# Kernel tuning notes

Measured on AMD Instinct MI355X. Metric: run time of the kernel, lower is better.

Reference implementation:

```python
import jax, jax.numpy as jnp
import numpy as np

K = 75        # kpoints
L = 8         # number of labels (output_dim)


def _knn_nonconformity(q, t, train_label, k=K, num_labels=L):
    """Brute-force kNN (Euclidean) + distance-weighted nonconformity.
    q: [B, D] queries; t: [N, D] train bank; train_label: [N] int.
    Returns [B, num_labels]: for each class i, sum of 1/dist over the k
    nearest neighbors whose label != i (0 weight for zero distance)."""
    # squared distances [B, N]
    d2 = (jnp.sum(q * q, axis=1, keepdims=True)
          - 2.0 * q @ t.T
          + jnp.sum(t * t, axis=1)[None, :])
    d2 = jnp.maximum(d2, 0.0)
    neg_top, idx = jax.lax.top_k(-d2, k)          # k smallest d2
    dist = jnp.sqrt(jnp.maximum(-neg_top, 0.0))    # [B, k]
    safe = jnp.where(dist > 0, dist, 1.0)
    w = jnp.where(dist > 0, 1.0 / safe, 0.0)       # [B, k]
    mismatch = 1.0 - jax.nn.one_hot(train_label[idx], num_labels, dtype=w.dtype)  # [B,k,L]
    return jnp.einsum('bk,bkl->bl', w, mismatch)


def setup_inputs() -> dict:
    key = jax.random.key(0)
    ks = jax.random.split(key, 12)
    B, N, D, H, C = 1024, 50000, 83, 128, 10000
    s = lambda fan_in: 1.0 / np.sqrt(fan_in)
    return {
        'x': jax.random.normal(ks[0], (B, D), jnp.float32),
        'train_x': jax.random.normal(ks[1], (N, D), jnp.float32),
        'train_label': jax.random.randint(ks[2], (N,), 0, L, jnp.int32),
        'cali': jax.random.uniform(ks[3], (C,), jnp.float32) * 50.0,
        'W1': jax.random.normal(ks[4], (D, H), jnp.float32) * s(D),
        'b1': jnp.zeros((H,), jnp.float32),
        'W2': jax.random.normal(ks[5], (H, H), jnp.float32) * s(H),
        'b2': jnp.zeros((H,), jnp.float32),
        'W3': jax.random.normal(ks[6], (H, H), jnp.float32) * s(H),
        'b3': jnp.zeros((H,), jnp.float32),
        'W4': jax.random.normal(ks[7], (H, L), jnp.float32) * s(H),
        'b4': jnp.zeros((L,), jnp.float32),
    }


def reference(x, train_x, train_label, cali, W1, b1, W2, b2, W3, b3, W4, b4):
    relu = jax.nn.relu
    # query-side MLP (inference: dropout inactive)
    h1 = relu(x @ W1 + b1)
    h2 = relu(h1 @ W2 + b2)
    h3 = relu(h2 @ W3 + b3)
    out = jax.nn.softmax(h3 @ W4 + b4, axis=-1)
    # train-side feature banks (what each kNTree was fit on)
    t1 = relu(train_x @ W1 + b1)
    t2 = relu(t1 @ W2 + b2)
    t3 = relu(t2 @ W3 + b3)
    t4 = jax.nn.softmax(t3 @ W4 + b4, axis=-1)
    # per-layer nonconformity [B, L], summed across the 5 layers
    total = (_knn_nonconformity(x, train_x, train_label)
             + _knn_nonconformity(h1, t1, train_label)
             + _knn_nonconformity(h2, t2, train_label)
             + _knn_nonconformity(h3, t3, train_label)
             + _knn_nonconformity(out, t4, train_label))
    # empirical p-value: fraction of calibration scores >= total nonconformity
    counts = jnp.sum(cali[None, None, :] >= total[:, :, None], axis=-1)  # [B, L]
    return counts.astype(jnp.float32) / cali.shape[0]
```

## Files before the change

### kernel.cpp

```cpp
#include <hip/hip_runtime.h>
#include <math.h>

#define KNN 75
#define NL 8
#define NB 1024
#define NT 50000
#define NT_PAD 50048
#define NCALI 10000
#define KC 32
#define TT 128
#define NTB 391
#define SLOTS 16
#define CAP 6144
#define NSUB 2048
#define NSB 16
#define SSTRIDE 24
#define SOFF 11
#define RSEL 32

#define PB_Q    384
#define PB_BANK 18750
#define PB_W1   48
#define PB_W23  64
#define PREP_BLOCKS (PB_Q+PB_BANK+PB_W1+2*PB_W23)

typedef __attribute__((ext_vector_type(8))) short bf16x8;
typedef __attribute__((ext_vector_type(4))) float f32x4;

__device__ __forceinline__ int swz(int c){ return c + ((c>>5)<<2); }

__device__ __forceinline__ unsigned short f2bf_rn(float x){
  unsigned u = __float_as_uint(x);
  unsigned r = (u + 0x7FFFu + ((u>>16)&1u)) >> 16;
  return (unsigned short)r;
}
__device__ __forceinline__ float bf2f(unsigned short h){
  return __uint_as_float(((unsigned)h)<<16);
}
__device__ __forceinline__ bf16x8 ld8(const unsigned short* p){
  return *(const bf16x8*)p;
}
__device__ __forceinline__ void gl_lds16(const unsigned short* g, unsigned short* l){
  __builtin_amdgcn_global_load_lds(
      (const __attribute__((address_space(1))) void*)g,
      (__attribute__((address_space(3))) void*)l, 16, 0, 0);
}

__device__ __forceinline__ void pad_one(const float* __restrict__ in,
                                        float* __restrict__ out, int M,
                                        int Din, int Dout, int idx){
  if (idx >= M*Dout) return;
  int r = idx / Dout, c = idx - r*Dout;
  out[idx] = (c < Din) ? in[r*Din + c] : 0.f;
}
__device__ __forceinline__ void wsplit_one(const float* __restrict__ W, int kreal,
                                           int dp, unsigned short* __restrict__ WtH,
                                           unsigned short* __restrict__ WtL, int idx){
  int n = idx / dp, k = idx - n*dp;
  float v = (k < kreal) ? W[(size_t)k*128 + n] : 0.f;
  unsigned short h = f2bf_rn(v);
  WtH[idx] = h;
  WtL[idx] = f2bf_rn(v - bf2f(h));
}
__global__ void prep_k(const float* __restrict__ x, float* __restrict__ xq0,
                       const float* __restrict__ txr, float* __restrict__ tbA,
                       const float* __restrict__ W1, unsigned short* wt1H, unsigned short* wt1L,
                       const float* __restrict__ W2, unsigned short* wt2H, unsigned short* wt2L,
                       const float* __restrict__ W3, unsigned short* wt3H, unsigned short* wt3L){
  int b = blockIdx.x, tid = threadIdx.x;
  if (b < PB_Q){
    pad_one(x, xq0, NB, 83, 96, b*256 + tid);
  } else if (b < PB_Q + PB_BANK){
    pad_one(txr, tbA, NT, 83, 96, (b-PB_Q)*256 + tid);
  } else if (b < PB_Q + PB_BANK + PB_W1){
    wsplit_one(W1, 83, 96,  wt1H, wt1L, (b-PB_Q-PB_BANK)*256 + tid);
  } else if (b < PB_Q + PB_BANK + PB_W1 + PB_W23){
    wsplit_one(W2, 128, 128, wt2H, wt2L, (b-PB_Q-PB_BANK-PB_W1)*256 + tid);
  } else {
    wsplit_one(W3, 128, 128, wt3H, wt3L, (b-PB_Q-PB_BANK-PB_W1-PB_W23)*256 + tid);
  }
}

__device__ __forceinline__ void qmlp_layer(
    const float* __restrict__ srcG, int lda,
    float (*H)[132], float (*As)[132], float (*Bs)[148],
    int kchunks, int kreal,
    const float* __restrict__ W, const float* __restrict__ bias,
    float* __restrict__ OutG, int rowBase, int tid)
{
  int r0 = (tid>>4)*8, c0 = (tid&15)*8;
  float acc[8][8];
  #pragma unroll
  for (int i=0;i<8;i++)
    #pragma unroll
    for (int j=0;j<8;j++) acc[i][j]=0.f;

  for (int kc=0;kc<kchunks;kc++){
    { int rr = tid>>3, k4=(tid&7)*4;
      #pragma unroll
      for (int i=0;i<4;i++){
        int row = rr + i*32;
        float4 v;
        if (srcG) v = *(const float4*)&srcG[(size_t)(rowBase+row)*lda + kc*KC + k4];
        else      v = *(const float4*)&H[row][kc*KC + k4];
        As[k4+0][row]=v.x; As[k4+1][row]=v.y; As[k4+2][row]=v.z; As[k4+3][row]=v.w;
      }
    }
    { int kk=tid>>5, c4=(tid&31)*4;
      #pragma unroll
      for (int i=0;i<4;i++){
        int k = kk + i*8, gk = kc*KC + k;
        float4 v = make_float4(0.f,0.f,0.f,0.f);
        if (gk < kreal) v = *(const float4*)&W[(size_t)gk*128 + c4];
        *(float4*)&Bs[k][swz(c4)] = v;
      }
    }
    __syncthreads();
    #pragma unroll 4
    for (int k=0;k<KC;k++){
      float4 a0 = *(const float4*)&As[k][r0];
      float4 a1 = *(const float4*)&As[k][r0+4];
      float4 b0 = *(const float4*)&Bs[k][swz(c0)];
      float4 b1 = *(const float4*)&Bs[k][swz(c0+4)];
      float av[8] = {a0.x,a0.y,a0.z,a0.w,a1.x,a1.y,a1.z,a1.w};
      float bv[8] = {b0.x,b0.y,b0.z,b0.w,b1.x,b1.y,b1.z,b1.w};
      #pragma unroll
      for (int i=0;i<8;i++)
        #pragma unroll
        for (int j=0;j<8;j++) acc[i][j] += av[i]*bv[j];
    }
    __syncthreads();
  }
  float bb[8];
  #pragma unroll
  for (int j=0;j<8;j++) bb[j]=bias[c0+j];
  #pragma unroll
  for (int i=0;i<8;i++){
    int row = r0 + i;
    float o[8];
    #pragma unroll
    for (int j=0;j<8;j++){ float v=acc[i][j]+bb[j]; o[j]=v>0.f?v:0.f; }
    *(float4*)&H[row][c0]   = make_float4(o[0],o[1],o[2],o[3]);
    *(float4*)&H[row][c0+4] = make_float4(o[4],o[5],o[6],o[7]);
    *(float4*)&OutG[(size_t)(rowBase+row)*128 + c0]   = make_float4(o[0],o[1],o[2],o[3]);
    *(float4*)&OutG[(size_t)(rowBase+row)*128 + c0+4] = make_float4(o[4],o[5],o[6],o[7]);
  }
  __syncthreads();
}

__global__ __launch_bounds__(256) void qmlp_k(
    const float* __restrict__ xq0,
    const float* __restrict__ W1, const float* __restrict__ b1,
    const float* __restrict__ W2, const float* __restrict__ b2,
    const float* __restrict__ W3, const float* __restrict__ b3,
    const float* __restrict__ W4, const float* __restrict__ b4,
    float* __restrict__ xq1, float* __restrict__ xq2, float* __restrict__ xq3,
    float* __restrict__ xq4)
{
  __shared__ float As[KC][132];
  __shared__ float Bs[KC][148];
  __shared__ float H[128][132];
  int tid = threadIdx.x;
  int rowBase = blockIdx.x*128;

  qmlp_layer(xq0, 96, H, As, Bs, 3, 83,  W1, b1, xq1, rowBase, tid);
  qmlp_layer(nullptr, 0, H, As, Bs, 4, 128, W2, b2, xq2, rowBase, tid);
  qmlp_layer(nullptr, 0, H, As, Bs, 4, 128, W3, b3, xq3, rowBase, tid);

  float* W4s = (float*)Bs;
  for (int i=tid;i<1024;i+=256) W4s[i]=W4[i];
  __syncthreads();
  if (tid < 128){
    int row = rowBase + tid;
    float v[8];
    #pragma unroll
    for (int c=0;c<8;c++) v[c]=b4[c];
    for (int k=0;k<128;k++){
      float a = H[tid][k];
      #pragma unroll
      for (int c=0;c<8;c++) v[c] += a*W4s[k*8+c];
    }
    float m=-1e30f;
    #pragma unroll
    for (int c=0;c<8;c++) m = v[c]>m ? v[c] : m;
    float s=0.f;
    #pragma unroll
    for (int c=0;c<8;c++){ v[c]=__expf(v[c]-m); s+=v[c]; }
    float inv=1.f/s;
    float* p = &xq4[(size_t)row*32];
    #pragma unroll
    for (int c=0;c<8;c++) p[c]=v[c]*inv;
    #pragma unroll
    for (int j=8;j<32;j++) p[j]=0.f;
  }
}

__global__ void mlp8sm_k(const float* __restrict__ A, const float* __restrict__ W4,
                         const float* __restrict__ b4, float* __restrict__ Out, int M){
  __shared__ float Ws[128*8];
  int tid = threadIdx.x;
  for (int i=tid;i<1024;i+=256) Ws[i]=W4[i];
  __syncthreads();
  int r = blockIdx.x*32 + (tid>>3), c = tid&7;
  if (r >= M) return;
  const float* a = &A[(size_t)r*128];
  float acc = b4[c];
  #pragma unroll 16
  for (int k=0;k<128;k++) acc += a[k]*Ws[k*8+c];
  int lane = tid & 63, base = lane & ~7;
  float v[8];
  #pragma unroll
  for (int j=0;j<8;j++) v[j] = __shfl(acc, base+j, 64);
  float m=-1e30f;
  #pragma unroll
  for (int j=0;j<8;j++) m = v[j]>m ? v[j] : m;
  float s=0.f;
  #pragma unroll
  for (int j=0;j<8;j++){ v[j]=__expf(v[j]-m); s+=v[j]; }
  float inv=1.f/s;
  float* p = &Out[(size_t)r*32];
  p[c]    = v[c]*inv;
  p[8+c]  = 0.f;
  p[16+c] = 0.f;
  p[24+c] = 0.f;
}

__global__ void conv_norm_k(
    const float* __restrict__ XA, unsigned short* __restrict__ HA,
    unsigned short* __restrict__ LA, float* __restrict__ nA, int MA,
    const float* __restrict__ XB, unsigned short* __restrict__ HB,
    unsigned short* __restrict__ LB, float* __restrict__ nB, int MB,
    int dp)
{
  int w = threadIdx.x>>6, lane = threadIdx.x&63;
  int row = blockIdx.x*4 + w;
  const float* src; unsigned short* dh; unsigned short* dl; float* nrm;
  if (row < MA){
    src=&XA[(size_t)row*dp]; dh=&HA[(size_t)row*dp]; dl=&LA[(size_t)row*dp]; nrm=&nA[row];
  } else {
    int r2 = row - MA;
    if (r2 >= MB) return;
    src=&XB[(size_t)r2*dp]; dh=&HB[(size_t)r2*dp]; dl=&LB[(size_t)r2*dp]; nrm=&nB[r2];
  }
  float s=0.f;
  for (int c=lane*2; c<dp; c+=128){
    float2 v = *(const float2*)&src[c];
    s += v.x*v.x + v.y*v.y;
    unsigned short h0 = f2bf_rn(v.x), h1 = f2bf_rn(v.y);
    float r0 = v.x - bf2f(h0), r1 = v.y - bf2f(h1);
    ushort2 hh; hh.x=h0; hh.y=h1;
    ushort2 ll; ll.x=f2bf_rn(r0); ll.y=f2bf_rn(r1);
    *(ushort2*)&dh[c]=hh;
    *(ushort2*)&dl[c]=ll;
  }
  #pragma unroll
  for (int off=32;off>0;off>>=1) s += __shfl_down(s, off, 64);
  if (lane==0) *nrm=s;
}

__device__ __forceinline__ void find_bin(int* hist, int* part, int nb, int Krem,
                                         int tid, int* s_B, int* s_lob){
  int ch = nb>>8;
  int base = tid*ch;
  int s=0;
  for (int b=base;b<base+ch;b++) s+=hist[b];
  int lane = tid & 63, wv = tid>>6;
  int v = s;
  #pragma unroll
  for (int off=1; off<64; off<<=1){
    int u = __shfl_up(v, off, 64);
    if (lane >= off) v += u;
  }
  if (lane==63) part[wv] = v;
  __syncthreads();
  int wbase = 0;
  #pragma unroll
  for (int w2=0; w2<4; w2++) wbase += (w2 < wv) ? part[w2] : 0;
  v += wbase;
  int excl = v - s;
  if (v >= Krem && excl < Krem){
    int lob = excl, B = base + ch - 1;
    for (int b=base;b<base+ch;b++){
      if (lob + hist[b] >= Krem){ B=b; break; }
      lob += hist[b];
    }
    *s_B = B; *s_lob = lob;
  }
  if (tid==255 && v < Krem){ *s_B = nb-1; *s_lob = 0; }
  __syncthreads();
}

__global__ __launch_bounds__(256) void sel64_k(const unsigned* __restrict__ skeys,
                                               unsigned* __restrict__ Tthr){
  __shared__ unsigned buf[NSUB];
  __shared__ int hist[2048];
  __shared__ int part[256];
  __shared__ int sB, sLob;
  int tid=threadIdx.x, q=blockIdx.x;
  for (int i=tid;i<NSUB;i+=256) buf[i]=skeys[(size_t)q*NSUB+i];
  int Krem=RSEL;
  for (int i=tid;i<2048;i+=256) hist[i]=0;
  __syncthreads();
  for (int i=tid;i<NSUB;i+=256) atomicAdd(&hist[buf[i]>>21],1);
  __syncthreads();
  find_bin(hist,part,2048,Krem,tid,&sB,&sLob);
  unsigned pre=(unsigned)sB; Krem-=sLob;
  for (int i=tid;i<2048;i+=256) hist[i]=0;
  __syncthreads();
  for (int i=tid;i<NSUB;i+=256){ unsigned k=buf[i]; if ((k>>21)==pre) atomicAdd(&hist[(k>>10)&0x7FFu],1); }
  __syncthreads();
  find_bin(hist,part,2048,Krem,tid,&sB,&sLob);
  pre=(pre<<11)|(unsigned)sB; Krem-=sLob;
  for (int i=tid;i<1024;i+=256) hist[i]=0;
  __syncthreads();
  for (int i=tid;i<NSUB;i+=256){ unsigned k=buf[i]; if ((k>>10)==pre) atomicAdd(&hist[k&0x3FFu],1); }
  __syncthreads();
  find_bin(hist,part,1024,Krem,tid,&sB,&sLob);
  if (tid==0) Tthr[q]=(pre<<10)|(unsigned)sB;
}

#define MFMA_SEC(BHC, BLC, AH, AL)                                               \
  _Pragma("unroll")                                                              \
  for (int tj=0;tj<8;tj++){                                                      \
    int rowB = tj*16 + col;                                                      \
    int sw = (((quad + (rowB>>1)) & 3) << 3);                                    \
    bf16x8 bh = *(const bf16x8*)&(BHC)[rowB*32 + sw];                            \
    bf16x8 bl = *(const bf16x8*)&(BLC)[rowB*32 + sw];                            \
    acc[tj] = __builtin_amdgcn_mfma_f32_16x16x32_bf16(AH, bh, acc[tj], 0,0,0);   \
    acc[tj] = __builtin_amdgcn_mfma_f32_16x16x32_bf16(AH, bl, acc[tj], 0,0,0);   \
    acc[tj] = __builtin_amdgcn_mfma_f32_16x16x32_bf16(AL, bh, acc[tj], 0,0,0);   \
  }

#define MFMA_KLOOP(ROWMAP)                                                       \
  size_t aoff = (size_t)(qbase + w*16 + col)*dp + quad*8;                        \
  const unsigned short* pAH = QH + aoff;                                         \
  const unsigned short* pAL = QL + aoff;                                         \
  int i0 = tid,      row0 = i0>>2, sg0 = ((i0&3) - (row0>>1)) & 3;               \
  int i1 = tid+256,  row1 = i1>>2, sg1 = ((i1&3) - (row1>>1)) & 3;               \
  size_t g0 = (size_t)(ROWMAP(n0+row0))*dp + (size_t)sg0*8;                      \
  size_t g1 = (size_t)(ROWMAP(n0+row1))*dp + (size_t)sg1*8;                      \
  f32x4 acc[8];                                                                  \
  _Pragma("unroll")                                                              \
  for (int tj=0;tj<8;tj++){ f32x4 z={0.f,0.f,0.f,0.f}; acc[tj]=z; }              \
  gl_lds16(TH + g0, BH0 + i0*8);                                                 \
  gl_lds16(TH + g1, BH0 + i1*8);                                                 \
  gl_lds16(TL + g0, BL0 + i0*8);                                                 \
  gl_lds16(TL + g1, BL0 + i1*8);                                                 \
  bf16x8 xh = ld8(pAH), xl = ld8(pAL);                                           \
  bf16x8 yh = xh, yl = xl;                                                       \
  _Pragma("unroll")                                                              \
  for (int kc=0; kc<kchunks; kc+=2){                                             \
    __syncthreads();                                                             \
    if (kc+1 < kchunks){                                                         \
      size_t ko=(size_t)(kc+1)*32;                                               \
      gl_lds16(TH + g0 + ko, BH1 + i0*8);                                        \
      gl_lds16(TH + g1 + ko, BH1 + i1*8);                                        \
      gl_lds16(TL + g0 + ko, BL1 + i0*8);                                        \
      gl_lds16(TL + g1 + ko, BL1 + i1*8);                                        \
      yh = ld8(pAH + ko); yl = ld8(pAL + ko);                                    \
    }                                                                            \
    MFMA_SEC(BH0, BL0, xh, xl);                                                  \
    if (kc+1 < kchunks){                                                         \
      __syncthreads();                                                           \
      if (kc+2 < kchunks){                                                       \
        size_t ko=(size_t)(kc+2)*32;                                             \
        gl_lds16(TH + g0 + ko, BH0 + i0*8);                                      \
        gl_lds16(TH + g1 + ko, BH0 + i1*8);                                      \
        gl_lds16(TL + g0 + ko, BL0 + i0*8);                                      \
        gl_lds16(TL + g1 + ko, BL0 + i1*8);                                      \
        xh = ld8(pAH + ko); xl = ld8(pAL + ko);                                  \
      }                                                                            \
      MFMA_SEC(BH1, BL1, yh, yl);                                                \
    }                                                                            \
  }

#define ROW_ID(r) (r)
#define ROW_SUB(r) ((r)*SSTRIDE + SOFF)

template<int KCH>
__global__ __launch_bounds__(256) void dist_mfma_k(
    const unsigned short* __restrict__ QH, const unsigned short* __restrict__ QL,
    const unsigned short* __restrict__ TH, const unsigned short* __restrict__ TL,
    const float* __restrict__ qn, const float* __restrict__ tn,
    const int* __restrict__ labels, const unsigned* __restrict__ Tthr,
    unsigned* __restrict__ slab)
{
  constexpr int dp = KCH*32;
  __shared__ __align__(16) unsigned short smem[4*4096];
  unsigned short* BH0 = smem;
  unsigned short* BH1 = smem + 4096;
  unsigned short* BL0 = smem + 8192;
  unsigned short* BL1 = smem + 12288;
  unsigned (*hitbuf)[SLOTS] = (unsigned (*)[SLOTS])smem;
  int* hcnt = (int*)(smem + 4096);
  int b = blockIdx.x;
  int xcd = b & 7, s = b >> 3;
  int qb = s & 15, tslot = s >> 4;
  int t_blk = xcd + 8*tslot;
  if (t_blk >= NTB) return;
  int tid = threadIdx.x, w = tid>>6, lane = tid&63;
  int quad = lane>>4, col = lane&15;
  int qbase = qb*64;
  int n0 = t_blk*TT;
  constexpr int kchunks = KCH;

  MFMA_KLOOP(ROW_ID)

  __syncthreads();
  if (tid<64) hcnt[tid]=0;
  __syncthreads();
  float qnr[4]; unsigned Tq[4]; float thrF[4];
  #pragma unroll
  for (int r=0;r<4;r++){
    int q = qbase + w*16 + quad*4 + r;
    qnr[r]  = qn[q];
    Tq[r]   = Tthr[q];
    thrF[r] = __uint_as_float(Tq[r] | 7u);
  }
  #pragma unroll
  for (int tj=0;tj<8;tj++){
    int t = n0 + tj*16 + col;
    if (t < NT){
      float tnv = tn[t];
      unsigned lab = (unsigned)labels[t];
      #pragma unroll
      for (int r=0;r<4;r++){
        float d2 = fmaf(-2.f, acc[tj][r], qnr[r] + tnv);
        if (d2 <= thrF[r]){
          float d2c = fmaxf(d2, 0.f);
          unsigned key = (__float_as_uint(d2c)&0xFFFFFFF8u) | lab;
          if (key < Tq[r]){
            int ql = w*16 + quad*4 + r;
            int idx = atomicAdd(&hcnt[ql], 1);
            if (idx < SLOTS-1) hitbuf[ql][1+idx] = key;
          }
        }
      }
    }
  }
  __syncthreads();
  if (tid<64) hitbuf[tid][0]=(unsigned)hcnt[tid];
  __syncthreads();
  {
    int q = tid>>2, sub = (tid&3)*4;
    uint4 v = *(uint4*)&hitbuf[q][sub];
    *(uint4*)&slab[((size_t)(qbase+q)*NTB + t_blk)*SLOTS + sub] = v;
  }
}

template<int KCH>
__global__ __launch_bounds__(256) void dist_sub_k(
    const unsigned short* __restrict__ QH, const unsigned short* __restrict__ QL,
    const unsigned short* __restrict__ TH, const unsigned short* __restrict__ TL,
    const float* __restrict__ qn, const float* __restrict__ tn,
    const int* __restrict__ labels, unsigned* __restrict__ keys)
{
  constexpr int dp = KCH*32;
  __shared__ __align__(16) unsigned short smem[4*4096];
  unsigned short* BH0 = smem;
  unsigned short* BH1 = smem + 4096;
  unsigned short* BL0 = smem + 8192;
  unsigned short* BL1 = smem + 12288;
  int b = blockIdx.x;
  int qb = b & 15, t_blk = b >> 4;
  int tid = threadIdx.x, w = tid>>6, lane = tid&63;
  int quad = lane>>4, col = lane&15;
  int qbase = qb*64;
  int n0 = t_blk*TT;
  constexpr int kchunks = KCH;

  MFMA_KLOOP(ROW_SUB)

  float qnr[4];
  #pragma unroll
  for (int r=0;r<4;r++)
    qnr[r] = qn[qbase + w*16 + quad*4 + r];
  #pragma unroll
  for (int tj=0;tj<8;tj++){
    int sI = n0 + tj*16 + col;
    int g  = sI*SSTRIDE + SOFF;
    float tnv = tn[g];
    unsigned lab = (unsigned)labels[g];
    #pragma unroll
    for (int r=0;r<4;r++){
      float d2 = fmaxf(fmaf(-2.f, acc[tj][r], qnr[r] + tnv), 0.f);
      unsigned key = (__float_as_uint(d2)&0xFFFFFFF8u) | lab;
      int q = qbase + w*16 + quad*4 + r;
      keys[(size_t)q*NSUB + sI] = key;
    }
  }
}

template<int KCH>
__global__ __launch_bounds__(256) void mlp_mfma_k(
    const unsigned short* __restrict__ QH, const unsigned short* __restrict__ QL,
    const unsigned short* __restrict__ TH, const unsigned short* __restrict__ TL,
    const float* __restrict__ bias, float* __restrict__ Out, int M)
{
  constexpr int dp = KCH*32;
  __shared__ __align__(16) unsigned short smem[4*4096];
  unsigned short* BH0 = smem;
  unsigned short* BH1 = smem + 4096;
  unsigned short* BL0 = smem + 8192;
  unsigned short* BL1 = smem + 12288;
  int tid = threadIdx.x, w = tid>>6, lane = tid&63;
  int quad = lane>>4, col = lane&15;
  int qbase = blockIdx.x*64;
  int n0 = 0;
  constexpr int kchunks = KCH;

  MFMA_KLOOP(ROW_ID)

  float bb[8];
  #pragma unroll
  for (int tj=0;tj<8;tj++) bb[tj] = bias[tj*16 + col];
  #pragma unroll
  for (int r=0;r<4;r++){
    int row = qbase + w*16 + quad*4 + r;
    if (row < M){
      #pragma unroll
      for (int tj=0;tj<8;tj++){
        float v = acc[tj][r] + bb[tj];
        Out[(size_t)row*128 + tj*16 + col] = v > 0.f ? v : 0.f;
      }
    }
  }
}

__global__ __launch_bounds__(256) void final_k(
    const unsigned* __restrict__ slab,
    const float* __restrict__ Qm, const float* __restrict__ Tm,
    const float* __restrict__ qn, const float* __restrict__ tn,
    const int* __restrict__ labels,
    float* __restrict__ tot, int first, int dp)
{
  __shared__ int hist[2048];
  __shared__ int part[256];
  __shared__ unsigned buf[CAP];
  __shared__ unsigned lowbuf[96];
  __shared__ float qrow[128];
  __shared__ int sB,sLob,s_cnt,s_low,s_bad;
  __shared__ float s_w[9];
  int tid=threadIdx.x, q=blockIdx.x;
  if (tid==0){ for (int j=0;j<9;j++) s_w[j]=0.f; s_cnt=0; s_low=0; s_bad=0; }
  __syncthreads();

  const unsigned* sq = slab + (size_t)q*NTB*SLOTS;
  for (int sidx=tid; sidx<NTB; sidx+=256){
    const unsigned* s = sq + (size_t)sidx*SLOTS;
    uint4 a = *(const uint4*)s;
    unsigned cnt = a.x;
    if (cnt > SLOTS-1){ s_bad=1; continue; }
    if (!cnt) continue;
    int base = atomicAdd(&s_cnt, (int)cnt);
    if (base + (int)cnt <= CAP){
      buf[base] = a.y;
      if (cnt>=2) buf[base+1] = a.z;
      if (cnt>=3) buf[base+2] = a.w;
      for (unsigned w=4; w<=cnt; w++) buf[base+w-1] = s[w];
    }
  }
  __syncthreads();
  int total = s_cnt;
  int bad = s_bad;

#define CONTRIB(kk) do{ float d2_=__uint_as_float((kk)&0xFFFFFFF8u); \
    if (d2_>0.f){ float w_=1.0f/sqrtf(d2_); \
      atomicAdd(&s_w[8],w_); atomicAdd(&s_w[(kk)&7u],w_); } }while(0)

  unsigned T; int Krem=KNN;
  if (!bad && total>=KNN && total<=CAP){
    for (int i=tid;i<2048;i+=256) hist[i]=0;
    __syncthreads();
    for (int i=tid;i<total;i+=256) atomicAdd(&hist[buf[i]>>21],1);
    __syncthreads();
    find_bin(hist,part,2048,Krem,tid,&sB,&sLob);
    unsigned pre=(unsigned)sB; Krem-=sLob;
    for (int i=tid;i<2048;i+=256) hist[i]=0;
    __syncthreads();
    for (int i=tid;i<total;i+=256){ unsigned k=buf[i]; if ((k>>21)==pre) atomicAdd(&hist[(k>>10)&0x7FFu],1); }
    __syncthreads();
    find_bin(hist,part,2048,Krem,tid,&sB,&sLob);
    pre=(pre<<11)|(unsigned)sB; Krem-=sLob;
    for (int i=tid;i<1024;i+=256) hist[i]=0;
    __syncthreads();
    for (int i=tid;i<total;i+=256){ unsigned k=buf[i]; if ((k>>10)==pre) atomicAdd(&hist[k&0x3FFu],1); }
    __syncthreads();
    find_bin(hist,part,1024,Krem,tid,&sB,&sLob);
    T=(pre<<10)|(unsigned)sB; Krem-=sLob;
    __syncthreads();
    for (int i=tid;i<total;i+=256){ unsigned k=buf[i]; if (k<T) CONTRIB(k); }
  } else {
    if (tid==0) s_cnt=0;
    for (int i=tid;i<dp;i+=256) qrow[i]=Qm[(size_t)q*dp+i];
    __syncthreads();
    float qq=qn[q];
    auto KEY=[&](int t)->unsigned{
      const float* br=&Tm[(size_t)t*dp];
      float dot=0.f;
      for (int k2=0;k2<dp;k2++) dot+=qrow[k2]*br[k2];
      float d2=fmaxf(qq-2.f*dot+tn[t],0.f);
      return (__float_as_uint(d2)&0xFFFFFFF8u)|(unsigned)labels[t];
    };
    for (int i=tid;i<2048;i+=256) hist[i]=0;
    __syncthreads();
    for (int t=tid;t<NT;t+=256) atomicAdd(&hist[KEY(t)>>21],1);
    __syncthreads();
    find_bin(hist,part,2048,Krem,tid,&sB,&sLob);
    int c=hist[sB]; Krem-=sLob;
    unsigned prefix=(unsigned)sB; int shift=21;
    if (c > CAP){
      __syncthreads();
      for (int i=tid;i<2048;i+=256) hist[i]=0;
      __syncthreads();
      for (int t=tid;t<NT;t+=256){ unsigned k=KEY(t); if ((k>>21)==prefix) atomicAdd(&hist[(k>>10)&0x7FFu],1); }
      __syncthreads();
      find_bin(hist,part,2048,Krem,tid,&sB,&sLob);
      c=hist[sB]; Krem-=sLob; prefix=(prefix<<11)|(unsigned)sB; shift=10;
    }
    if (c > CAP){
      __syncthreads();
      for (int i=tid;i<1024;i+=256) hist[i]=0;
      __syncthreads();
      for (int t=tid;t<NT;t+=256){ unsigned k=KEY(t); if ((k>>10)==prefix) atomicAdd(&hist[k&0x3FFu],1); }
      __syncthreads();
      find_bin(hist,part,1024,Krem,tid,&sB,&sLob);
      c=hist[sB]; Krem-=sLob; prefix=(prefix<<10)|(unsigned)sB; shift=0;
    }
    if (c <= CAP){
      for (int t=tid;t<NT;t+=256){
        unsigned k=KEY(t); unsigned pp=k>>shift;
        if (pp==prefix){ int j=atomicAdd(&s_cnt,1); if (j<CAP) buf[j]=k; }
        else if (pp<prefix){ int j=atomicAdd(&s_low,1); if (j<96) lowbuf[j]=k; }
      }
      __syncthreads();
      int sh=shift;
      while (sh>0){
        int nsh=(sh==21)?10:0;
        int nb=1<<(sh-nsh);
        __syncthreads();
        for (int i=tid;i<nb;i+=256) hist[i]=0;
        __syncthreads();
        int cc=s_cnt;
        for (int i=tid;i<cc;i+=256) atomicAdd(&hist[(buf[i]>>nsh)&(unsigned)(nb-1)],1);
        __syncthreads();
        find_bin(hist,part,nb,Krem,tid,&sB,&sLob);
        Krem-=sLob; prefix=(prefix<<(sh-nsh))|(unsigned)sB; sh=nsh;
      }
      T=prefix;
      __syncthreads();
      int lowc=s_low, cc=s_cnt;
      for (int i=tid;i<lowc;i+=256){ unsigned k=lowbuf[i]; CONTRIB(k); }
      for (int i=tid;i<cc;i+=256){ unsigned k=buf[i]; if (k<T) CONTRIB(k); }
    } else {
      T=prefix;
      for (int t=tid;t<NT;t+=256){ unsigned k=KEY(t); if (k<T) CONTRIB(k); }
    }
  }
  __syncthreads();
  if (tid==0){
    float d2=__uint_as_float(T&0xFFFFFFF8u);
    float w=(d2>0.f)?(1.0f/sqrtf(d2)):0.f;
    s_w[8] += (float)Krem*w;
    s_w[T&7u] += (float)Krem*w;
  }
  __syncthreads();
  if (tid<8){
    float contrib = s_w[8]-s_w[tid];
    size_t o=(size_t)q*NL+tid;
    tot[o] = first ? contrib : tot[o]+contrib;
  }
#undef CONTRIB
}

__global__ void pvalue_k(const float* __restrict__ tot, const float* __restrict__ cali,
                         float* __restrict__ out){
  __shared__ float t8[NL];
  __shared__ int part[4][NL];
  int tid=threadIdx.x, q=blockIdx.x;
  if (tid<NL) t8[tid]=tot[(size_t)q*NL+tid];
  __syncthreads();
  float th[NL];
  #pragma unroll
  for (int c=0;c<NL;c++) th[c]=t8[c];
  int cnt[NL];
  #pragma unroll
  for (int c=0;c<NL;c++) cnt[c]=0;
  for (int i=tid;i<NCALI;i+=256){
    float v=cali[i];
    #pragma unroll
    for (int c=0;c<NL;c++) cnt[c] += (v>=th[c]) ? 1 : 0;
  }
  #pragma unroll
  for (int c=0;c<NL;c++){
    #pragma unroll
    for (int off=32;off>0;off>>=1) cnt[c]+=__shfl_down(cnt[c],off,64);
  }
  if ((tid&63)==0){
    #pragma unroll
    for (int c=0;c<NL;c++) part[tid>>6][c]=cnt[c];
  }
  __syncthreads();
  if (tid<NL){
    int s=part[0][tid]+part[1][tid]+part[2][tid]+part[3][tid];
    out[(size_t)q*NL+tid] = (float)s / 10000.f;
  }
}

template<int KCH>
static void knn_layer(const float* Qm, const float* Bank, float* qnl, int first,
                      const int* lbl, float* tnb,
                      unsigned short* qH, unsigned short* qL,
                      unsigned short* bankH, unsigned short* bankL,
                      unsigned* skeys, unsigned* sT, unsigned* slab,
                      float* tot, hipStream_t stream){
  constexpr int dp = KCH*32;
  conv_norm_k<<<(NT+NB)/4,256,0,stream>>>(Bank, bankH, bankL, tnb, NT,
                                          Qm, qH, qL, qnl, NB, dp);
  dist_sub_k<KCH><<<16*NSB,256,0,stream>>>(qH,qL,bankH,bankL,qnl,tnb,lbl,skeys);
  sel64_k<<<NB,256,0,stream>>>(skeys,sT);
  dist_mfma_k<KCH><<<8*16*49,256,0,stream>>>(qH,qL,bankH,bankL,qnl,tnb,lbl,sT,slab);
  final_k<<<NB,256,0,stream>>>(slab,Qm,Bank,qnl,tnb,lbl,tot,first,dp);
}

extern "C" void kernel_launch(void* const* d_in, const int* in_sizes, int n_in,
                              void* d_out, int out_size, void* d_ws, size_t ws_size,
                              hipStream_t stream) {
  const float* x   = (const float*)d_in[0];
  const float* txr = (const float*)d_in[1];
  const int*   lbl = (const int*)  d_in[2];
  const float* cal = (const float*)d_in[3];
  const float* W1  = (const float*)d_in[4];
  const float* b1  = (const float*)d_in[5];
  const float* W2  = (const float*)d_in[6];
  const float* b2  = (const float*)d_in[7];
  const float* W3  = (const float*)d_in[8];
  const float* b3  = (const float*)d_in[9];
  const float* W4  = (const float*)d_in[10];
  const float* b4  = (const float*)d_in[11];
  float* out = (float*)d_out;
  float* ws  = (float*)d_ws;

  size_t off=0;
  float* xq0=ws+off; off+=(size_t)NB*96;
  float* xq1=ws+off; off+=(size_t)NB*128;
  float* xq2=ws+off; off+=(size_t)NB*128;
  float* xq3=ws+off; off+=(size_t)NB*128;
  float* xq4=ws+off; off+=(size_t)NB*32;
  float* tbA=ws+off; off+=(size_t)NT*128;
  float* tbB=ws+off; off+=(size_t)NT*128;
  float* tb4=ws+off; off+=(size_t)NT*32;
  float* qnb=ws+off; off+=(size_t)5*NB;
  float* tnb=ws+off; off+=(size_t)NT;
  float* tot=ws+off; off+=(size_t)NB*NL;
  unsigned* sT=(unsigned*)(ws+off); off+=NB;
  unsigned short* qH=(unsigned short*)(ws+off); off+=(size_t)NB*64;
  unsigned short* qL=(unsigned short*)(ws+off); off+=(size_t)NB*64;
  unsigned short* bankH=(unsigned short*)(ws+off); off+=(size_t)NT_PAD*64;
  unsigned short* bankL=(unsigned short*)(ws+off); off+=(size_t)NT_PAD*64;
  unsigned short* wt1H=(unsigned short*)(ws+off); off+=(size_t)128*48;
  unsigned short* wt1L=(unsigned short*)(ws+off); off+=(size_t)128*48;
  unsigned short* wt2H=(unsigned short*)(ws+off); off+=(size_t)128*64;
  unsigned short* wt2L=(unsigned short*)(ws+off); off+=(size_t)128*64;
  unsigned short* wt3H=(unsigned short*)(ws+off); off+=(size_t)128*64;
  unsigned short* wt3L=(unsigned short*)(ws+off); off+=(size_t)128*64;
  off=(off+3)&~(size_t)3;
  unsigned* slab=(unsigned*)(ws+off);
  unsigned* skeys=(unsigned*)(ws+off);
  { size_t slab_sz=(size_t)NB*NTB*SLOTS, skey_sz=(size_t)NB*NSUB;
    off += (slab_sz > skey_sz ? slab_sz : skey_sz); }

  prep_k<<<PREP_BLOCKS,256,0,stream>>>(x,xq0,txr,tbA,
                                       W1,wt1H,wt1L,W2,wt2H,wt2L,W3,wt3H,wt3L);
  qmlp_k<<<8,256,0,stream>>>(xq0,W1,b1,W2,b2,W3,b3,W4,b4,xq1,xq2,xq3,xq4);

  knn_layer<3>(xq0, tbA, qnb+0*NB, 1, lbl, tnb, qH,qL,bankH,bankL, skeys,sT,slab, tot, stream);
  mlp_mfma_k<3><<<2*NTB,256,0,stream>>>(bankH,bankL,wt1H,wt1L,b1,tbB,NT);
  knn_layer<4>(xq1, tbB, qnb+1*NB, 0, lbl, tnb, qH,qL,bankH,bankL, skeys,sT,slab, tot, stream);
  mlp_mfma_k<4><<<2*NTB,256,0,stream>>>(bankH,bankL,wt2H,wt2L,b2,tbA,NT);
  knn_layer<4>(xq2, tbA, qnb+2*NB, 0, lbl, tnb, qH,qL,bankH,bankL, skeys,sT,slab, tot, stream);
  mlp_mfma_k<4><<<2*NTB,256,0,stream>>>(bankH,bankL,wt3H,wt3L,b3,tbB,NT);
  knn_layer<4>(xq3, tbB, qnb+3*NB, 0, lbl, tnb, qH,qL,bankH,bankL, skeys,sT,slab, tot, stream);
  mlp8sm_k<<<(NT+31)/32,256,0,stream>>>(tbB,W4,b4,tb4,NT);
  knn_layer<1>(xq4, tb4, qnb+4*NB, 0, lbl, tnb, qH,qL,bankH,bankL, skeys,sT,slab, tot, stream);

  pvalue_k<<<NB,256,0,stream>>>(tot,cal,out);
}
```

Before: 727.7 us.

## Fuse bf16 hi/lo split and norms into MLP epilogues, drop per-layer conversion

The per-layer conv_norm_k pass is removed from the kNN pipeline. The query-side MLP kernel and the bank-side MLP kernels (mlp_mfma_k, mlp8sm_k) now write the bf16 high/low split and the squared row norms directly in their epilogues. Bank splits are double-buffered so a layer can read one buffer while the next layer's split is written to the other. Only the first layer still runs a standalone conversion. This saves four full passes over the 50k-row bank plus the extra launches, in exchange for more stores and a shuffle reduction in the MLP epilogues and extra workspace.

```diff
diff --git a/kernel.cpp b/kernel.cpp
--- a/kernel.cpp
+++ b/kernel.cpp
@@ -148,6 +148,25 @@
   __syncthreads();
 }
 
+__device__ __forceinline__ void qsplit(float (*H)[132],
+                                       unsigned short* __restrict__ qh,
+                                       unsigned short* __restrict__ ql,
+                                       float* __restrict__ qn,
+                                       int rowBase, int tid){
+  if (tid < 128){
+    int gr = rowBase + tid;
+    float s = 0.f;
+    for (int k=0;k<128;k++){
+      float v = H[tid][k];
+      s += v*v;
+      unsigned short h = f2bf_rn(v);
+      qh[(size_t)gr*128 + k] = h;
+      ql[(size_t)gr*128 + k] = f2bf_rn(v - bf2f(h));
+    }
+    qn[gr] = s;
+  }
+}
+
 __global__ __launch_bounds__(256) void qmlp_k(
     const float* __restrict__ xq0,
     const float* __restrict__ W1, const float* __restrict__ b1,
@@ -155,7 +174,12 @@
     const float* __restrict__ W3, const float* __restrict__ b3,
     const float* __restrict__ W4, const float* __restrict__ b4,
     float* __restrict__ xq1, float* __restrict__ xq2, float* __restrict__ xq3,
-    float* __restrict__ xq4)
+    float* __restrict__ xq4,
+    unsigned short* qH1, unsigned short* qL1,
+    unsigned short* qH2, unsigned short* qL2,
+    unsigned short* qH3, unsigned short* qL3,
+    unsigned short* qH4, unsigned short* qL4,
+    float* __restrict__ qnb)
 {
   __shared__ float As[KC][132];
   __shared__ float Bs[KC][148];
@@ -164,8 +188,11 @@
   int rowBase = blockIdx.x*128;
 
   qmlp_layer(xq0, 96, H, As, Bs, 3, 83,  W1, b1, xq1, rowBase, tid);
+  qsplit(H, qH1, qL1, qnb+1*NB, rowBase, tid);
   qmlp_layer(nullptr, 0, H, As, Bs, 4, 128, W2, b2, xq2, rowBase, tid);
+  qsplit(H, qH2, qL2, qnb+2*NB, rowBase, tid);
   qmlp_layer(nullptr, 0, H, As, Bs, 4, 128, W3, b3, xq3, rowBase, tid);
+  qsplit(H, qH3, qL3, qnb+3*NB, rowBase, tid);
 
   float* W4s = (float*)Bs;
   for (int i=tid;i<1024;i+=256) W4s[i]=W4[i];
@@ -188,15 +215,26 @@
     for (int c=0;c<8;c++){ v[c]=__expf(v[c]-m); s+=v[c]; }
     float inv=1.f/s;
     float* p = &xq4[(size_t)row*32];
-    #pragma unroll
-    for (int c=0;c<8;c++) p[c]=v[c]*inv;
-    #pragma unroll
-    for (int j=8;j<32;j++) p[j]=0.f;
+    float nn=0.f;
+    #pragma unroll
+    for (int c=0;c<8;c++){
+      float pv = v[c]*inv;
+      p[c]=pv;
+      nn += pv*pv;
+      unsigned short h = f2bf_rn(pv);
+      qH4[(size_t)row*32 + c] = h;
+      qL4[(size_t)row*32 + c] = f2bf_rn(pv - bf2f(h));
+    }
+    #pragma unroll
+    for (int j=8;j<32;j++){ p[j]=0.f; qH4[(size_t)row*32+j]=0; qL4[(size_t)row*32+j]=0; }
+    qnb[4*NB + row] = nn;
   }
 }
 
 __global__ void mlp8sm_k(const float* __restrict__ A, const float* __restrict__ W4,
-                         const float* __restrict__ b4, float* __restrict__ Out, int M){
+                         const float* __restrict__ b4, float* __restrict__ Out,
+                         unsigned short* __restrict__ SH, unsigned short* __restrict__ SL,
+                         float* __restrict__ nrm, int M){
   __shared__ float Ws[128*8];
   int tid = threadIdx.x;
   for (int i=tid;i<1024;i+=256) Ws[i]=W4[i];
@@ -218,11 +256,22 @@
   #pragma unroll
   for (int j=0;j<8;j++){ v[j]=__expf(v[j]-m); s+=v[j]; }
   float inv=1.f/s;
+  float nn=0.f;
+  #pragma unroll
+  for (int j=0;j<8;j++){ float pv=v[j]*inv; v[j]=pv; nn+=pv*pv; }
   float* p = &Out[(size_t)r*32];
-  p[c]    = v[c]*inv;
+  float pv = v[c];
+  p[c]    = pv;
   p[8+c]  = 0.f;
   p[16+c] = 0.f;
   p[24+c] = 0.f;
+  unsigned short h = f2bf_rn(pv);
+  SH[(size_t)r*32 + c]    = h;
+  SL[(size_t)r*32 + c]    = f2bf_rn(pv - bf2f(h));
+  SH[(size_t)r*32 + 8+c]  = 0; SL[(size_t)r*32 + 8+c]  = 0;
+  SH[(size_t)r*32 + 16+c] = 0; SL[(size_t)r*32 + 16+c] = 0;
+  SH[(size_t)r*32 + 24+c] = 0; SL[(size_t)r*32 + 24+c] = 0;
+  if (c==0) nrm[r] = nn;
 }
 
 __global__ void conv_norm_k(
@@ -369,7 +418,7 @@
         gl_lds16(TL + g0 + ko, BL0 + i0*8);                                      \
         gl_lds16(TL + g1 + ko, BL0 + i1*8);                                      \
         xh = ld8(pAH + ko); xl = ld8(pAL + ko);                                  \
-      }                                                                            \
+      }                                                                          \
       MFMA_SEC(BH1, BL1, yh, yl);                                                \
     }                                                                            \
   }
@@ -495,7 +544,9 @@
 __global__ __launch_bounds__(256) void mlp_mfma_k(
     const unsigned short* __restrict__ QH, const unsigned short* __restrict__ QL,
     const unsigned short* __restrict__ TH, const unsigned short* __restrict__ TL,
-    const float* __restrict__ bias, float* __restrict__ Out, int M)
+    const float* __restrict__ bias, float* __restrict__ Out,
+    unsigned short* __restrict__ SH, unsigned short* __restrict__ SL,
+    float* __restrict__ nrm, int M)
 {
   constexpr int dp = KCH*32;
   __shared__ __align__(16) unsigned short smem[4*4096];
@@ -518,10 +569,23 @@
   for (int r=0;r<4;r++){
     int row = qbase + w*16 + quad*4 + r;
     if (row < M){
+      float vv[8]; float s=0.f;
       #pragma unroll
       for (int tj=0;tj<8;tj++){
         float v = acc[tj][r] + bb[tj];
-        Out[(size_t)row*128 + tj*16 + col] = v > 0.f ? v : 0.f;
+        v = v > 0.f ? v : 0.f;
+        vv[tj] = v;
+        s += v*v;
+        Out[(size_t)row*128 + tj*16 + col] = v;
+      }
+      #pragma unroll
+      for (int off=1; off<16; off<<=1) s += __shfl_xor(s, off, 16);
+      if (col==0) nrm[row] = s;
+      #pragma unroll
+      for (int tj=0;tj<8;tj++){
+        unsigned short h = f2bf_rn(vv[tj]);
+        SH[(size_t)row*128 + tj*16 + col] = h;
+        SL[(size_t)row*128 + tj*16 + col] = f2bf_rn(vv[tj] - bf2f(h));
       }
     }
   }
@@ -708,18 +772,16 @@
 }
 
 template<int KCH>
-static void knn_layer(const float* Qm, const float* Bank, float* qnl, int first,
-                      const int* lbl, float* tnb,
-                      unsigned short* qH, unsigned short* qL,
-                      unsigned short* bankH, unsigned short* bankL,
+static void knn_layer(const float* Qm, const float* Bank,
+                      const unsigned short* qh, const unsigned short* ql, float* qnl,
+                      const unsigned short* bkH, const unsigned short* bkL,
+                      int first, const int* lbl, float* tnb,
                       unsigned* skeys, unsigned* sT, unsigned* slab,
                       float* tot, hipStream_t stream){
   constexpr int dp = KCH*32;
-  conv_norm_k<<<(NT+NB)/4,256,0,stream>>>(Bank, bankH, bankL, tnb, NT,
-                                          Qm, qH, qL, qnl, NB, dp);
-  dist_sub_k<KCH><<<16*NSB,256,0,stream>>>(qH,qL,bankH,bankL,qnl,tnb,lbl,skeys);
+  dist_sub_k<KCH><<<16*NSB,256,0,stream>>>(qh,ql,bkH,bkL,qnl,tnb,lbl,skeys);
   sel64_k<<<NB,256,0,stream>>>(skeys,sT);
-  dist_mfma_k<KCH><<<8*16*49,256,0,stream>>>(qH,qL,bankH,bankL,qnl,tnb,lbl,sT,slab);
+  dist_mfma_k<KCH><<<8*16*49,256,0,stream>>>(qh,ql,bkH,bkL,qnl,tnb,lbl,sT,slab);
   final_k<<<NB,256,0,stream>>>(slab,Qm,Bank,qnl,tnb,lbl,tot,first,dp);
 }
 
@@ -754,10 +816,20 @@
   float* tnb=ws+off; off+=(size_t)NT;
   float* tot=ws+off; off+=(size_t)NB*NL;
   unsigned* sT=(unsigned*)(ws+off); off+=NB;
-  unsigned short* qH=(unsigned short*)(ws+off); off+=(size_t)NB*64;
-  unsigned short* qL=(unsigned short*)(ws+off); off+=(size_t)NB*64;
-  unsigned short* bankH=(unsigned short*)(ws+off); off+=(size_t)NT_PAD*64;
-  unsigned short* bankL=(unsigned short*)(ws+off); off+=(size_t)NT_PAD*64;
+  unsigned short* qH0=(unsigned short*)(ws+off); off+=(size_t)NB*48;
+  unsigned short* qL0=(unsigned short*)(ws+off); off+=(size_t)NB*48;
+  unsigned short* qH1=(unsigned short*)(ws+off); off+=(size_t)NB*64;
+  unsigned short* qL1=(unsigned short*)(ws+off); off+=(size_t)NB*64;
+  unsigned short* qH2=(unsigned short*)(ws+off); off+=(size_t)NB*64;
+  unsigned short* qL2=(unsigned short*)(ws+off); off+=(size_t)NB*64;
+  unsigned short* qH3=(unsigned short*)(ws+off); off+=(size_t)NB*64;
+  unsigned short* qL3=(unsigned short*)(ws+off); off+=(size_t)NB*64;
+  unsigned short* qH4=(unsigned short*)(ws+off); off+=(size_t)NB*16;
+  unsigned short* qL4=(unsigned short*)(ws+off); off+=(size_t)NB*16;
+  unsigned short* bkAH=(unsigned short*)(ws+off); off+=(size_t)NT_PAD*64;
+  unsigned short* bkAL=(unsigned short*)(ws+off); off+=(size_t)NT_PAD*64;
+  unsigned short* bkBH=(unsigned short*)(ws+off); off+=(size_t)NT_PAD*64;
+  unsigned short* bkBL=(unsigned short*)(ws+off); off+=(size_t)NT_PAD*64;
   unsigned short* wt1H=(unsigned short*)(ws+off); off+=(size_t)128*48;
   unsigned short* wt1L=(unsigned short*)(ws+off); off+=(size_t)128*48;
   unsigned short* wt2H=(unsigned short*)(ws+off); off+=(size_t)128*64;
@@ -772,17 +844,20 @@
 
   prep_k<<<PREP_BLOCKS,256,0,stream>>>(x,xq0,txr,tbA,
                                        W1,wt1H,wt1L,W2,wt2H,wt2L,W3,wt3H,wt3L);
-  qmlp_k<<<8,256,0,stream>>>(xq0,W1,b1,W2,b2,W3,b3,W4,b4,xq1,xq2,xq3,xq4);
-
-  knn_layer<3>(xq0, tbA, qnb+0*NB, 1, lbl, tnb, qH,qL,bankH,bankL, skeys,sT,slab, tot, stream);
-  mlp_mfma_k<3><<<2*NTB,256,0,stream>>>(bankH,bankL,wt1H,wt1L,b1,tbB,NT);
-  knn_layer<4>(xq1, tbB, qnb+1*NB, 0, lbl, tnb, qH,qL,bankH,bankL, skeys,sT,slab, tot, stream);
-  mlp_mfma_k<4><<<2*NTB,256,0,stream>>>(bankH,bankL,wt2H,wt2L,b2,tbA,NT);
-  knn_layer<4>(xq2, tbA, qnb+2*NB, 0, lbl, tnb, qH,qL,bankH,bankL, skeys,sT,slab, tot, stream);
-  mlp_mfma_k<4><<<2*NTB,256,0,stream>>>(bankH,bankL,wt3H,wt3L,b3,tbB,NT);
-  knn_layer<4>(xq3, tbB, qnb+3*NB, 0, lbl, tnb, qH,qL,bankH,bankL, skeys,sT,slab, tot, stream);
-  mlp8sm_k<<<(NT+31)/32,256,0,stream>>>(tbB,W4,b4,tb4,NT);
-  knn_layer<1>(xq4, tb4, qnb+4*NB, 0, lbl, tnb, qH,qL,bankH,bankL, skeys,sT,slab, tot, stream);
+  qmlp_k<<<8,256,0,stream>>>(xq0,W1,b1,W2,b2,W3,b3,W4,b4,xq1,xq2,xq3,xq4,
+                             qH1,qL1,qH2,qL2,qH3,qL3,qH4,qL4,qnb);
+  conv_norm_k<<<(NT+NB)/4,256,0,stream>>>(tbA, bkAH, bkAL, tnb, NT,
+                                          xq0, qH0, qL0, qnb+0*NB, NB, 96);
+
+  knn_layer<3>(xq0, tbA, qH0,qL0, qnb+0*NB, bkAH,bkAL, 1, lbl, tnb, skeys,sT,slab, tot, stream);
+  mlp_mfma_k<3><<<2*NTB,256,0,stream>>>(bkAH,bkAL,wt1H,wt1L,b1,tbB,bkBH,bkBL,tnb,NT);
+  knn_layer<4>(xq1, tbB, qH1,qL1, qnb+1*NB, bkBH,bkBL, 0, lbl, tnb, skeys,sT,slab, tot, stream);
+  mlp_mfma_k<4><<<2*NTB,256,0,stream>>>(bkBH,bkBL,wt2H,wt2L,b2,tbA,bkAH,bkAL,tnb,NT);
+  knn_layer<4>(xq2, tbA, qH2,qL2, qnb+2*NB, bkAH,bkAL, 0, lbl, tnb, skeys,sT,slab, tot, stream);
+  mlp_mfma_k<4><<<2*NTB,256,0,stream>>>(bkAH,bkAL,wt3H,wt3L,b3,tbB,bkBH,bkBL,tnb,NT);
+  knn_layer<4>(xq3, tbB, qH3,qL3, qnb+3*NB, bkBH,bkBL, 0, lbl, tnb, skeys,sT,slab, tot, stream);
+  mlp8sm_k<<<(NT+31)/32,256,0,stream>>>(tbB,W4,b4,tb4,bkAH,bkAL,tnb,NT);
+  knn_layer<1>(xq4, tb4, qH4,qL4, qnb+4*NB, bkAH,bkAL, 0, lbl, tnb, skeys,sT,slab, tot, stream);
 
   pvalue_k<<<NB,256,0,stream>>>(tot,cal,out);
 }
```

After: 725.8 us. About the same (-0.3%).
